# Kernel optimization log

Hardware: AMD Instinct MI355X
Metric: run time of the kernel (lower is better)

Reference implementation:

```python
import jax, jax.numpy as jnp
import numpy as np

B, L, NC, REG_MAX = 32, 8400, 15, 16
EPS_IOU = 0.1  # RotatedIoULoss eps (clamp min)


def _cross2(a, b):
    return a[..., 0] * b[..., 1] - a[..., 1] * b[..., 0]


def _box2corners(box):
    # box [...,5] = (x, y, w, h, alpha) -> corners [...,4,2], consistent cyclic order
    x, y, w, h, a = (box[..., i] for i in range(5))
    xo = jnp.array([0.5, -0.5, -0.5, 0.5], box.dtype)
    yo = jnp.array([-0.5, -0.5, 0.5, 0.5], box.dtype)
    px = w[..., None] * xo  # [...,4]
    py = h[..., None] * yo
    c, s = jnp.cos(a)[..., None], jnp.sin(a)[..., None]
    rx = c * px - s * py + x[..., None]
    ry = s * px + c * py + y[..., None]
    return jnp.stack([rx, ry], axis=-1)


def _box_intersection(c1, c2):
    # segment-segment intersections between the 4 edges of each box -> [N,16,2], valid [N,16]
    p1 = c1[:, :, None, :]
    p2 = jnp.roll(c1, -1, axis=-2)[:, :, None, :]
    q1 = c2[:, None, :, :]
    q2 = jnp.roll(c2, -1, axis=-2)[:, None, :, :]
    d1, d2, r = p2 - p1, q2 - q1, q1 - p1
    den = _cross2(d1, d2)
    safe = jnp.where(jnp.abs(den) < 1e-12, jnp.ones_like(den), den)
    t = _cross2(r, d2) / safe
    u = _cross2(r, d1) / safe
    valid = (jnp.abs(den) > 1e-12) & (t > 0) & (t < 1) & (u > 0) & (u < 1)
    pts = p1 + t[..., None] * d1
    pts = jnp.where(valid[..., None], pts, jnp.zeros_like(pts))
    N = c1.shape[0]
    return pts.reshape(N, 16, 2), valid.reshape(N, 16)


def _points_in_box(pts, corners):
    # pts [N,4,2] inside rotated box given by corners [N,4,2] (projection test)
    a = corners[:, 0:1]
    ab = corners[:, 1:2] - a
    ad = corners[:, 3:4] - a
    ap = pts - a
    pab = jnp.sum(ap * ab, -1)
    pad = jnp.sum(ap * ad, -1)
    nab = jnp.sum(ab * ab, -1)
    nad = jnp.sum(ad * ad, -1)
    return (pab >= 0) & (pab <= nab) & (pad >= 0) & (pad <= nad)


def _sorted_poly_area(verts, mask):
    # sort candidate vertices CCW around the centroid of valid ones, shoelace area
    mf = mask.astype(verts.dtype)
    nv = jnp.maximum(mf.sum(-1, keepdims=True), 1.0)  # [N,1]
    mean = (verts * mf[..., None]).sum(-2, keepdims=True) / nv[..., None]
    rel = verts - mean
    ang = jnp.where(mask, jnp.arctan2(rel[..., 1], rel[..., 0]), 1e6)
    order = jnp.argsort(ang, axis=-1)
    sv = jnp.take_along_axis(verts, order[..., None], axis=-2)
    sm = jnp.take_along_axis(mask, order, axis=-1)
    sv = jnp.where(sm[..., None], sv, sv[..., :1, :])  # pad invalid with first vertex
    nxt = jnp.roll(sv, -1, axis=-2)
    return 0.5 * jnp.abs(jnp.sum(sv[..., 0] * nxt[..., 1] - nxt[..., 0] * sv[..., 1], axis=-1))


def diff_iou_rotated_2d(box1, box2):
    # box1, box2: [N,5] -> iou [N]
    c1, c2 = _box2corners(box1), _box2corners(box2)
    ipts, ivalid = _box_intersection(c1, c2)
    m1 = _points_in_box(c1, c2)
    m2 = _points_in_box(c2, c1)
    verts = jnp.concatenate([c1, c2, ipts], axis=-2)   # [N,24,2]
    mask = jnp.concatenate([m1, m2, ivalid], axis=-1)  # [N,24]
    inter = _sorted_poly_area(verts, mask)
    area1 = box1[..., 2] * box1[..., 3]
    area2 = box2[..., 2] * box2[..., 3]
    return inter / (area1 + area2 - inter + 1e-9)


def setup_inputs() -> dict:
    key = jax.random.key(0)
    ks = jax.random.split(key, 8)
    wh_off = jnp.array([0.0, 0.0, 0.2, 0.2], jnp.float32)
    pred_bboxes = jax.random.uniform(ks[0], (B, L, 4), jnp.float32) + wh_off
    target_bboxes = jax.random.uniform(ks[1], (B, L, 4), jnp.float32) + wh_off
    pred_angles = 0.5 * jax.random.normal(ks[2], (B, L, 1), jnp.float32)      # radians
    target_angles = 90.0 * jax.random.uniform(ks[3], (B, L, 1), jnp.float32)  # degrees
    pred_dist = jax.random.normal(ks[4], (B, L, (REG_MAX + 1) * 4), jnp.float32)
    target_scores = jax.random.uniform(ks[5], (B, L, NC), jnp.float32)
    fg_mask = jax.random.bernoulli(ks[6], 0.25, (B, L))
    tss = jnp.sum(target_scores.sum(-1) * fg_mask.astype(jnp.float32))[None]
    anchor_points = jax.random.uniform(ks[7], (L, 2), jnp.float32)
    return {"pred_dist": pred_dist, "pred_bboxes": pred_bboxes, "pred_angles": pred_angles,
            "anchor_points": anchor_points, "target_bboxes": target_bboxes,
            "target_angles": target_angles, "target_scores": target_scores,
            "target_scores_sum": tss, "fg_mask": fg_mask}


def reference(pred_dist, pred_bboxes, pred_angles, anchor_points, target_bboxes,
              target_angles, target_scores, target_scores_sum, fg_mask):
    mf = fg_mask.astype(pred_bboxes.dtype).reshape(-1)          # [B*L]
    num_pos = mf.sum()
    pi = jnp.asarray(np.pi, pred_bboxes.dtype)
    pred_R = jnp.concatenate([pred_bboxes, pred_angles], -1).reshape(-1, 5)
    tgt_R = jnp.concatenate([target_bboxes, target_angles / 180.0 * pi], -1).reshape(-1, 5)
    ious = jnp.maximum(diff_iou_rotated_2d(pred_R, tgt_R), EPS_IOU)  # clamp(min=eps)
    bbox_weight = target_scores.sum(-1).reshape(-1)             # [B*L]
    loss_elem = (1.0 - ious) * bbox_weight * mf                 # masked per-anchor loss
    lsum = loss_elem.sum()
    lmean = lsum / jnp.maximum(num_pos, 1.0)
    loss_iou = jnp.where(target_scores_sum[0] == 0, lsum, lmean)
    loss_iou = jnp.where(num_pos > 0, loss_iou, 0.0)
    loss_dfl = pred_dist.sum() * 0.0
    return (loss_iou, loss_dfl)
```

## Files before the change

### kernel.cpp

```cpp
#include <hip/hip_runtime.h>
#include <math.h>

#define NCLS 15
#define NV 24
#define EPB 1024


#define CSWAP(A, B)                                                       \
    {                                                                     \
        const float ka = ang[A], kb = ang[B];                             \
        const bool sw = kb < ka;                                          \
        ang[A] = sw ? kb : ka; ang[B] = sw ? ka : kb;                     \
        const float xa = vx[A], xb = vx[B];                               \
        vx[A] = sw ? xb : xa; vx[B] = sw ? xa : xb;                       \
        const float ya = vy[A], yb = vy[B];                               \
        vy[A] = sw ? yb : ya; vy[B] = sw ? ya : yb;                       \
    }

__device__ __forceinline__ float elem_loss(
    int i,
    const float* __restrict__ pred_bboxes,
    const float* __restrict__ pred_angles,
    const float* __restrict__ target_bboxes,
    const float* __restrict__ target_angles,
    const float* __restrict__ target_scores)
{
    const float4 pb = reinterpret_cast<const float4*>(pred_bboxes)[i];
    const float4 tb = reinterpret_cast<const float4*>(target_bboxes)[i];
    const float pa = pred_angles[i];
    const float ta = (target_angles[i] / 180.0f) * (float)M_PI;

    float c1x[4], c1y[4], c2x[4], c2y[4];
    {
        const float xo[4] = { 0.5f, -0.5f, -0.5f, 0.5f };
        const float yo[4] = { -0.5f, -0.5f, 0.5f, 0.5f };
        float cs = cosf(pa), sn = sinf(pa);
#pragma unroll
        for (int k = 0; k < 4; ++k) {
            const float px = pb.z * xo[k], py = pb.w * yo[k];
            c1x[k] = cs * px - sn * py + pb.x;
            c1y[k] = sn * px + cs * py + pb.y;
        }
        cs = cosf(ta); sn = sinf(ta);
#pragma unroll
        for (int k = 0; k < 4; ++k) {
            const float px = tb.z * xo[k], py = tb.w * yo[k];
            c2x[k] = cs * px - sn * py + tb.x;
            c2y[k] = sn * px + cs * py + tb.y;
        }
    }

    float vx[NV], vy[NV];
    bool  vm[NV];

    {
        const float ax = c2x[0], ay = c2y[0];
        const float abx = c2x[1] - ax, aby = c2y[1] - ay;
        const float adx = c2x[3] - ax, ady = c2y[3] - ay;
        const float nab = abx * abx + aby * aby;
        const float nad = adx * adx + ady * ady;
#pragma unroll
        for (int k = 0; k < 4; ++k) {
            const float apx = c1x[k] - ax, apy = c1y[k] - ay;
            const float pab = apx * abx + apy * aby;
            const float pad = apx * adx + apy * ady;
            vx[k] = c1x[k]; vy[k] = c1y[k];
            vm[k] = (pab >= 0.0f) && (pab <= nab) && (pad >= 0.0f) && (pad <= nad);
        }
    }
    {
        const float ax = c1x[0], ay = c1y[0];
        const float abx = c1x[1] - ax, aby = c1y[1] - ay;
        const float adx = c1x[3] - ax, ady = c1y[3] - ay;
        const float nab = abx * abx + aby * aby;
        const float nad = adx * adx + ady * ady;
#pragma unroll
        for (int k = 0; k < 4; ++k) {
            const float apx = c2x[k] - ax, apy = c2y[k] - ay;
            const float pab = apx * abx + apy * aby;
            const float pad = apx * adx + apy * ady;
            vx[4 + k] = c2x[k]; vy[4 + k] = c2y[k];
            vm[4 + k] = (pab >= 0.0f) && (pab <= nab) && (pad >= 0.0f) && (pad <= nad);
        }
    }
#pragma unroll
    for (int a = 0; a < 4; ++a) {
        const float p1x = c1x[a], p1y = c1y[a];
        const float d1x = c1x[(a + 1) & 3] - p1x;
        const float d1y = c1y[(a + 1) & 3] - p1y;
#pragma unroll
        for (int b = 0; b < 4; ++b) {
            const float q1x = c2x[b], q1y = c2y[b];
            const float d2x = c2x[(b + 1) & 3] - q1x;
            const float d2y = c2y[(b + 1) & 3] - q1y;
            const float rx = q1x - p1x, ry = q1y - p1y;
            const float den = d1x * d2y - d1y * d2x;
            const float safe = (fabsf(den) < 1e-12f) ? 1.0f : den;
            const float t = (rx * d2y - ry * d2x) / safe;
            const float u = (rx * d1y - ry * d1x) / safe;
            const bool val = (fabsf(den) > 1e-12f) &&
                             (t > 0.0f) && (t < 1.0f) &&
                             (u > 0.0f) && (u < 1.0f);
            const int idx = 8 + a * 4 + b;
            vx[idx] = val ? (p1x + t * d1x) : 0.0f;
            vy[idx] = val ? (p1y + t * d1y) : 0.0f;
            vm[idx] = val;
        }
    }

    float sx = 0.0f, sy = 0.0f, nvf = 0.0f;
#pragma unroll
    for (int k = 0; k < NV; ++k) {
        sx  += vm[k] ? vx[k] : 0.0f;
        sy  += vm[k] ? vy[k] : 0.0f;
        nvf += vm[k] ? 1.0f : 0.0f;
    }
    const float nv = fmaxf(nvf, 1.0f);
    const float mx = sx / nv, my = sy / nv;

    float ang[NV];
#pragma unroll
    for (int k = 0; k < NV; ++k) {
        const float rx = vx[k] - mx, ry = vy[k] - my;
        const float d = fabsf(rx) + fabsf(ry);
        const float a = rx / d;
        float p = (ry >= 0.0f) ? (1.0f - a) : (3.0f + a);
        if (d == 0.0f) p = 0.0f;
        ang[k] = vm[k] ? p : INFINITY;
    }

#pragma unroll
    for (int p = 1; p < 32; p <<= 1) {
#pragma unroll
        for (int k = p; k >= 1; k >>= 1) {
#pragma unroll
            for (int jj = k & (p - 1); jj + k < 32; jj += 2 * k) {
#pragma unroll
                for (int ii = 0; ii < k; ++ii) {
                    if (ii + jj + k < 32 &&
                        ((ii + jj) / (2 * p)) == ((ii + jj + k) / (2 * p))) {
                        if (ii + jj + k < NV) {
                            CSWAP(ii + jj, ii + jj + k);
                        }
                    }
                }
            }
        }
    }

    const float v0x = vx[0], v0y = vy[0];
    float total = 0.0f;
#pragma unroll
    for (int k = 0; k < NV; ++k) {
        const bool vk = ang[k] < INFINITY;
        const bool vn = (k < NV - 1) ? (ang[k + 1] < INFINITY) : false;
        const float nx = vn ? vx[k + 1] : v0x;
        const float ny = vn ? vy[k + 1] : v0y;
        total += vk ? (vx[k] * ny - nx * vy[k]) : 0.0f;
    }
    const float inter = 0.5f * fabsf(total);

    const float area1 = pb.z * pb.w;
    const float area2 = tb.z * tb.w;
    float iou = inter / (area1 + area2 - inter + 1e-9f);
    iou = fmaxf(iou, 0.1f);

    float w = 0.0f;
    const float* sp = target_scores + (size_t)i * NCLS;
#pragma unroll
    for (int k = 0; k < NCLS; ++k) w += sp[k];

    return (1.0f - iou) * w;
}

__global__ __launch_bounds__(256) void fused_loss_kernel(
    const float* __restrict__ pred_bboxes,
    const float* __restrict__ pred_angles,
    const float* __restrict__ target_bboxes,
    const float* __restrict__ target_angles,
    const float* __restrict__ target_scores,
    const int*   __restrict__ fg_mask,
    const float* __restrict__ tss,
    float* __restrict__ ws,
    float* __restrict__ out,
    int n, int nblocks)
{
    __shared__ int sidx[EPB];
    __shared__ int scnt;
    __shared__ float sl[4];
    __shared__ bool slast;

    const int tid = threadIdx.x;
    if (tid == 0) scnt = 0;
    __syncthreads();

    const int base = blockIdx.x * EPB + tid * 4;
    if (base < n) {
        const int4 m = *reinterpret_cast<const int4*>(fg_mask + base);
        if (m.x) sidx[atomicAdd(&scnt, 1)] = base + 0;
        if (m.y) sidx[atomicAdd(&scnt, 1)] = base + 1;
        if (m.z) sidx[atomicAdd(&scnt, 1)] = base + 2;
        if (m.w) sidx[atomicAdd(&scnt, 1)] = base + 3;
    }
    __syncthreads();
    const int lcnt = scnt;

    float loss = 0.0f;
    for (int k = tid; k < lcnt; k += 256)
        loss += elem_loss(sidx[k], pred_bboxes, pred_angles,
                          target_bboxes, target_angles, target_scores);

#pragma unroll
    for (int off = 32; off > 0; off >>= 1)
        loss += __shfl_down(loss, off, 64);
    const int lane = tid & 63;
    const int wid  = tid >> 6;
    if (lane == 0) sl[wid] = loss;
    __syncthreads();
    if (tid == 0) {
        atomicAdd(&ws[0], sl[0] + sl[1] + sl[2] + sl[3]);
        atomicAdd((int*)ws + 1, lcnt);
        __threadfence();
        const int done = atomicAdd((int*)ws + 2, 1);
        slast = (done == nblocks - 1);
    }
    __syncthreads();

    if (slast && tid == 0) {
        const float lsum = atomicAdd(&ws[0], 0.0f);
        const float npos = (float)atomicAdd((int*)ws + 1, 0);
        const float lmean = lsum / fmaxf(npos, 1.0f);
        float li = (tss[0] == 0.0f) ? lsum : lmean;
        li = (npos > 0.0f) ? li : 0.0f;
        out[0] = li;
        out[1] = 0.0f;
    }
}

extern "C" void kernel_launch(void* const* d_in, const int* in_sizes, int n_in,
                              void* d_out, int out_size, void* d_ws, size_t ws_size,
                              hipStream_t stream) {
    const float* pred_bboxes   = (const float*)d_in[1];
    const float* pred_angles   = (const float*)d_in[2];
    const float* target_bboxes = (const float*)d_in[4];
    const float* target_angles = (const float*)d_in[5];
    const float* target_scores = (const float*)d_in[6];
    const float* tss           = (const float*)d_in[7];
    const int*   fg_mask       = (const int*)d_in[8];

    float* ws  = (float*)d_ws;
    float* out = (float*)d_out;

    const int n = in_sizes[8];
    const int blocks = (n + EPB - 1) / EPB;

    hipMemsetAsync(d_ws, 0, 16, stream);
    fused_loss_kernel<<<blocks, 256, 0, stream>>>(
        pred_bboxes, pred_angles, target_bboxes, target_angles,
        target_scores, fg_mask, tss, ws, out, n, blocks);
}
```

Before: 145.7 us.

## Use cooperative grid sync with fixed 256 blocks instead of atomics and memset

```diff
diff --git a/kernel.cpp b/kernel.cpp
--- a/kernel.cpp
+++ b/kernel.cpp
@@ -1,9 +1,14 @@
 #include <hip/hip_runtime.h>
+#include <hip/hip_cooperative_groups.h>
 #include <math.h>
+
+namespace cg = cooperative_groups;
 
 #define NCLS 15
 #define NV 24
-#define EPB 1024
+#define NB 256
+#define BT 256
+#define MAXEPB 1280
 
 
 #define CSWAP(A, B)                                                       \
@@ -173,7 +178,7 @@
     return (1.0f - iou) * w;
 }
 
-__global__ __launch_bounds__(256) void fused_loss_kernel(
+__global__ __launch_bounds__(BT) void fused_loss_coop_kernel(
     const float* __restrict__ pred_bboxes,
     const float* __restrict__ pred_angles,
     const float* __restrict__ target_bboxes,
@@ -183,30 +188,27 @@
     const float* __restrict__ tss,
     float* __restrict__ ws,
     float* __restrict__ out,
-    int n, int nblocks)
+    int n, int epb)
 {
-    __shared__ int sidx[EPB];
+    __shared__ int sidx[MAXEPB];
     __shared__ int scnt;
     __shared__ float sl[4];
-    __shared__ bool slast;
 
     const int tid = threadIdx.x;
     if (tid == 0) scnt = 0;
     __syncthreads();
 
-    const int base = blockIdx.x * EPB + tid * 4;
-    if (base < n) {
-        const int4 m = *reinterpret_cast<const int4*>(fg_mask + base);
-        if (m.x) sidx[atomicAdd(&scnt, 1)] = base + 0;
-        if (m.y) sidx[atomicAdd(&scnt, 1)] = base + 1;
-        if (m.z) sidx[atomicAdd(&scnt, 1)] = base + 2;
-        if (m.w) sidx[atomicAdd(&scnt, 1)] = base + 3;
+    const int base = blockIdx.x * epb;
+    for (int e = tid; e < epb; e += BT) {
+        const int g = base + e;
+        if (g < n && fg_mask[g] != 0)
+            sidx[atomicAdd(&scnt, 1)] = g;
     }
     __syncthreads();
     const int lcnt = scnt;
 
     float loss = 0.0f;
-    for (int k = tid; k < lcnt; k += 256)
+    for (int k = tid; k < lcnt; k += BT)
         loss += elem_loss(sidx[k], pred_bboxes, pred_angles,
                           target_bboxes, target_angles, target_scores);
 
@@ -218,22 +220,32 @@
     if (lane == 0) sl[wid] = loss;
     __syncthreads();
     if (tid == 0) {
-        atomicAdd(&ws[0], sl[0] + sl[1] + sl[2] + sl[3]);
-        atomicAdd((int*)ws + 1, lcnt);
-        __threadfence();
-        const int done = atomicAdd((int*)ws + 2, 1);
-        slast = (done == nblocks - 1);
-    }
-    __syncthreads();
-
-    if (slast && tid == 0) {
-        const float lsum = atomicAdd(&ws[0], 0.0f);
-        const float npos = (float)atomicAdd((int*)ws + 1, 0);
-        const float lmean = lsum / fmaxf(npos, 1.0f);
-        float li = (tss[0] == 0.0f) ? lsum : lmean;
-        li = (npos > 0.0f) ? li : 0.0f;
-        out[0] = li;
-        out[1] = 0.0f;
+        ws[blockIdx.x] = sl[0] + sl[1] + sl[2] + sl[3];
+        ((int*)ws)[NB + blockIdx.x] = lcnt;
+    }
+
+    cg::this_grid().sync();
+
+    if (blockIdx.x == 0) {
+        float l = atomicAdd(&ws[tid], 0.0f);
+        float c = (float)atomicAdd((int*)ws + NB + tid, 0);
+#pragma unroll
+        for (int off = 32; off > 0; off >>= 1) {
+            l += __shfl_down(l, off, 64);
+            c += __shfl_down(c, off, 64);
+        }
+        __shared__ float fl[4], fc[4];
+        if (lane == 0) { fl[wid] = l; fc[wid] = c; }
+        __syncthreads();
+        if (tid == 0) {
+            const float lsum = fl[0] + fl[1] + fl[2] + fl[3];
+            const float npos = fc[0] + fc[1] + fc[2] + fc[3];
+            const float lmean = lsum / fmaxf(npos, 1.0f);
+            float li = (tss[0] == 0.0f) ? lsum : lmean;
+            li = (npos > 0.0f) ? li : 0.0f;
+            out[0] = li;
+            out[1] = 0.0f;
+        }
     }
 }
 
@@ -251,11 +263,14 @@
     float* ws  = (float*)d_ws;
     float* out = (float*)d_out;
 
-    const int n = in_sizes[8];
-    const int blocks = (n + EPB - 1) / EPB;
-
-    hipMemsetAsync(d_ws, 0, 16, stream);
-    fused_loss_kernel<<<blocks, 256, 0, stream>>>(
-        pred_bboxes, pred_angles, target_bboxes, target_angles,
-        target_scores, fg_mask, tss, ws, out, n, blocks);
+    int n   = in_sizes[8];
+    int epb = (n + NB - 1) / NB;
+
+    void* args[] = {
+        (void*)&pred_bboxes, (void*)&pred_angles, (void*)&target_bboxes,
+        (void*)&target_angles, (void*)&target_scores, (void*)&fg_mask,
+        (void*)&tss, (void*)&ws, (void*)&out, (void*)&n, (void*)&epb
+    };
+    hipLaunchCooperativeKernel((void*)fused_loss_coop_kernel,
+                               dim3(NB), dim3(BT), args, 0, stream);
 }
```

Measured after the change: 188.6 us. 29.4% more time.
